# Kernel tuning notes

Measured on AMD Instinct MI355X. Metric: run time of the kernel, lower is better.

## Reference

```python
import jax, jax.numpy as jnp
import numpy as np

TOPK = 0.5

def setup_inputs() -> dict:
    key = jax.random.key(0)
    k1, k2 = jax.random.split(key)
    B, C, H, W = 32, 512, 64, 64
    inputs = jax.random.normal(k1, (B, C, H, W), dtype=jnp.float32)
    targets = jax.random.normal(k2, (B, C, H, W), dtype=jnp.float32)
    return {"inputs": inputs, "targets": targets}

def reference(inputs, targets):
    B, C = targets.shape[0], targets.shape[1]
    # L2 norm over spatial dims -> [B, C]
    norm = jnp.sqrt(jnp.sum(targets * targets, axis=(-1, -2)))
    k = int(TOPK * C)
    # indices of top-k channels by norm (descending), per batch element
    _, idx_keep = jax.lax.top_k(norm, k)  # [B, k]
    # scatter ones into mask at kept channel indices
    mask = jnp.zeros((B, C), dtype=inputs.dtype)
    mask = mask.at[jnp.arange(B)[:, None], idx_keep].set(1.0)
    # squared diff, spatial mean -> [B, C]
    sq_diff = (inputs - targets) ** 2
    spatial_reduced = jnp.mean(sq_diff, axis=(-1, -2))
    masked_loss = spatial_reduced * mask
    return jnp.sum(masked_loss) / jnp.sum(mask)
```

## Files before the change

kernel.cpp:

```cpp
#include <hip/hip_runtime.h>

#define B 32
#define C 512
#define HW 4096
#define K 256

__inline__ __device__ float wave_reduce(float v) {
    #pragma unroll
    for (int o = 32; o > 0; o >>= 1) v += __shfl_down(v, o, 64);
    return v;
}

__global__ __launch_bounds__(256) void plane_reduce(
        const float* __restrict__ in, const float* __restrict__ tgt,
        float* __restrict__ norm2, float* __restrict__ ssd) {
    const int plane = blockIdx.x;
    const size_t base = (size_t)plane * HW;
    const float4* __restrict__ in4 = (const float4*)(in  + base);
    const float4* __restrict__ tg4 = (const float4*)(tgt + base);

    float t2 = 0.f, d2 = 0.f;
    #pragma unroll
    for (int i = 0; i < 4; ++i) {
        const int j = threadIdx.x + i * 256;
        const float4 a = in4[j];
        const float4 t = tg4[j];
        const float dx = a.x - t.x, dy = a.y - t.y, dz = a.z - t.z, dw = a.w - t.w;
        t2 += t.x * t.x + t.y * t.y + t.z * t.z + t.w * t.w;
        d2 += dx * dx + dy * dy + dz * dz + dw * dw;
    }

    t2 = wave_reduce(t2);
    d2 = wave_reduce(d2);

    __shared__ float st[4], sd[4];
    const int lane = threadIdx.x & 63, wid = threadIdx.x >> 6;
    if (lane == 0) { st[wid] = t2; sd[wid] = d2; }
    __syncthreads();
    if (threadIdx.x == 0) {
        norm2[plane] = st[0] + st[1] + st[2] + st[3];
        ssd[plane]   = sd[0] + sd[1] + sd[2] + sd[3];
    }
}

__global__ __launch_bounds__(C) void topk_mask_sum(
        const float* __restrict__ norm2, const float* __restrict__ ssd,
        float* __restrict__ bsum) {
    __shared__ float sn[C];
    __shared__ float red[C / 64];
    const int b = blockIdx.x, c = threadIdx.x;
    sn[c] = norm2[b * C + c];
    __syncthreads();

    const float my = sn[c];
    int rank = 0;
    #pragma unroll 8
    for (int j = 0; j < C; ++j) {
        const float o = sn[j];
        rank += (o > my) || (o == my && j < c);
    }
    float v = (rank < K) ? ssd[b * C + c] : 0.f;

    v = wave_reduce(v);
    const int lane = c & 63, wid = c >> 6;
    if (lane == 0) red[wid] = v;
    __syncthreads();
    if (c < 64) {
        float r = (c < C / 64) ? red[c] : 0.f;
        r = wave_reduce(r);
        if (c == 0) bsum[b] = r;
    }
}

__global__ __launch_bounds__(64) void finalize(
        const float* __restrict__ bsum, float* __restrict__ out) {
    float v = (threadIdx.x < B) ? bsum[threadIdx.x] : 0.f;
    v = wave_reduce(v);
    if (threadIdx.x == 0)
        out[0] = v / ((float)HW * (float)(B * K));
}

extern "C" void kernel_launch(void* const* d_in, const int* in_sizes, int n_in,
                              void* d_out, int out_size, void* d_ws, size_t ws_size,
                              hipStream_t stream) {
    const float* in  = (const float*)d_in[0];
    const float* tgt = (const float*)d_in[1];
    float* out = (float*)d_out;

    float* norm2 = (float*)d_ws;
    float* ssd   = norm2 + B * C;
    float* bsum  = ssd + B * C;

    plane_reduce<<<B * C, 256, 0, stream>>>(in, tgt, norm2, ssd);
    topk_mask_sum<<<B, C, 0, stream>>>(norm2, ssd, bsum);
    finalize<<<1, 64, 0, stream>>>(bsum, out);
}
```

Before: 510.4 us.

## Select top-k channels first, then compute squared diff only on kept planes

Splits the work into three kernels: a target-only norm pass, a top-k selection that writes kept channel indices, and a masked squared-difference pass over only the selected planes that accumulates into the output with atomics. The intent is to skip the input reads and the difference arithmetic for discarded channels. The catch is that kept target planes must be read a second time, so total DRAM traffic stays about the same unless those planes are still in cache. It also adds scattered plane access, atomic accumulation with nondeterministic summation order, and a hardcoded scale constant.

```diff
diff --git a/kernel.cpp b/kernel.cpp
--- a/kernel.cpp
+++ b/kernel.cpp
@@ -4,6 +4,9 @@
 #define C 512
 #define HW 4096
 #define K 256
+#define INV_SCALE (1.f / 33554432.f)
+
+typedef float f4_t __attribute__((ext_vector_type(4)));
 
 __inline__ __device__ float wave_reduce(float v) {
     #pragma unroll
@@ -11,47 +14,32 @@
     return v;
 }
 
-__global__ __launch_bounds__(256) void plane_reduce(
-        const float* __restrict__ in, const float* __restrict__ tgt,
-        float* __restrict__ norm2, float* __restrict__ ssd) {
+__global__ __launch_bounds__(256) void norm_pass(
+        const float* __restrict__ tgt, float* __restrict__ norm2) {
     const int plane = blockIdx.x;
-    const size_t base = (size_t)plane * HW;
-    const float4* __restrict__ in4 = (const float4*)(in  + base);
-    const float4* __restrict__ tg4 = (const float4*)(tgt + base);
-
-    float t2 = 0.f, d2 = 0.f;
+    const float4* __restrict__ tg4 = (const float4*)(tgt + (size_t)plane * HW);
+    float t2 = 0.f;
     #pragma unroll
     for (int i = 0; i < 4; ++i) {
-        const int j = threadIdx.x + i * 256;
-        const float4 a = in4[j];
-        const float4 t = tg4[j];
-        const float dx = a.x - t.x, dy = a.y - t.y, dz = a.z - t.z, dw = a.w - t.w;
+        const float4 t = tg4[threadIdx.x + i * 256];
         t2 += t.x * t.x + t.y * t.y + t.z * t.z + t.w * t.w;
-        d2 += dx * dx + dy * dy + dz * dz + dw * dw;
     }
-
+    __shared__ float s4[4];
     t2 = wave_reduce(t2);
-    d2 = wave_reduce(d2);
-
-    __shared__ float st[4], sd[4];
     const int lane = threadIdx.x & 63, wid = threadIdx.x >> 6;
-    if (lane == 0) { st[wid] = t2; sd[wid] = d2; }
+    if (lane == 0) s4[wid] = t2;
     __syncthreads();
-    if (threadIdx.x == 0) {
-        norm2[plane] = st[0] + st[1] + st[2] + st[3];
-        ssd[plane]   = sd[0] + sd[1] + sd[2] + sd[3];
-    }
+    if (threadIdx.x == 0) norm2[plane] = s4[0] + s4[1] + s4[2] + s4[3];
 }
 
-__global__ __launch_bounds__(C) void topk_mask_sum(
-        const float* __restrict__ norm2, const float* __restrict__ ssd,
-        float* __restrict__ bsum) {
+__global__ __launch_bounds__(C) void topk_select(
+        const float* __restrict__ norm2, int* __restrict__ keep,
+        float* __restrict__ out) {
     __shared__ float sn[C];
-    __shared__ float red[C / 64];
     const int b = blockIdx.x, c = threadIdx.x;
     sn[c] = norm2[b * C + c];
+    if (b == 0 && c == 0) out[0] = 0.f;
     __syncthreads();
-
     const float my = sn[c];
     int rank = 0;
     #pragma unroll 8
@@ -59,25 +47,34 @@
         const float o = sn[j];
         rank += (o > my) || (o == my && j < c);
     }
-    float v = (rank < K) ? ssd[b * C + c] : 0.f;
-
-    v = wave_reduce(v);
-    const int lane = c & 63, wid = c >> 6;
-    if (lane == 0) red[wid] = v;
-    __syncthreads();
-    if (c < 64) {
-        float r = (c < C / 64) ? red[c] : 0.f;
-        r = wave_reduce(r);
-        if (c == 0) bsum[b] = r;
-    }
+    if (rank < K) keep[b * K + rank] = c;
 }
 
-__global__ __launch_bounds__(64) void finalize(
-        const float* __restrict__ bsum, float* __restrict__ out) {
-    float v = (threadIdx.x < B) ? bsum[threadIdx.x] : 0.f;
-    v = wave_reduce(v);
+__global__ __launch_bounds__(256) void masked_ssd(
+        const float* __restrict__ in, const float* __restrict__ tgt,
+        const int* __restrict__ keep, float* __restrict__ out) {
+    const int i = blockIdx.x;
+    const int b = i >> 8;
+    const int c = keep[i];
+    const size_t base = (size_t)(b * C + c) * HW;
+    const f4_t* __restrict__ in4 = (const f4_t*)(in + base);
+    const float4* __restrict__ tg4 = (const float4*)(tgt + base);
+    float d2 = 0.f;
+    #pragma unroll
+    for (int k = 0; k < 4; ++k) {
+        const int j = threadIdx.x + k * 256;
+        const f4_t  a = __builtin_nontemporal_load(in4 + j);
+        const float4 t = tg4[j];
+        const float dx = a.x - t.x, dy = a.y - t.y, dz = a.z - t.z, dw = a.w - t.w;
+        d2 += dx * dx + dy * dy + dz * dz + dw * dw;
+    }
+    __shared__ float s4[4];
+    d2 = wave_reduce(d2);
+    const int lane = threadIdx.x & 63, wid = threadIdx.x >> 6;
+    if (lane == 0) s4[wid] = d2;
+    __syncthreads();
     if (threadIdx.x == 0)
-        out[0] = v / ((float)HW * (float)(B * K));
+        atomicAdd(out, (s4[0] + s4[1] + s4[2] + s4[3]) * INV_SCALE);
 }
 
 extern "C" void kernel_launch(void* const* d_in, const int* in_sizes, int n_in,
@@ -88,10 +85,9 @@
     float* out = (float*)d_out;
 
     float* norm2 = (float*)d_ws;
-    float* ssd   = norm2 + B * C;
-    float* bsum  = ssd + B * C;
+    int*   keep  = (int*)(norm2 + B * C);
 
-    plane_reduce<<<B * C, 256, 0, stream>>>(in, tgt, norm2, ssd);
-    topk_mask_sum<<<B, C, 0, stream>>>(norm2, ssd, bsum);
-    finalize<<<1, 64, 0, stream>>>(bsum, out);
+    norm_pass<<<B * C, 256, 0, stream>>>(tgt, norm2);
+    topk_select<<<B, C, 0, stream>>>(norm2, keep, out);
+    masked_ssd<<<B * K, 256, 0, stream>>>(in, tgt, keep, out);
 }
```

Measured after the change: 571.8 us. 1.12x slower.
